# Performance work log

Hardware: AMD Instinct MI355X
Metric: run time of the kernel (lower is better)

Reference implementation:

```python
import jax, jax.numpy as jnp
import numpy as np

ALPHA = 0.5
SMOOTH = 1e-05
ITERS = 10


def _max_pool3x3(x):
    # 3x3 max pool, stride 1, SAME padding on NCHW tensor
    return jax.lax.reduce_window(
        x, -jnp.inf, jax.lax.max,
        window_dimensions=(1, 1, 3, 3),
        window_strides=(1, 1, 1, 1),
        padding='SAME')


def _soft_erode(x):
    return -_max_pool3x3(-x)


def _soft_dilate(x):
    return _max_pool3x3(x)


def _soft_skeletonize(img, iterations=ITERS):
    def body(skel, _):
        eroded = _soft_erode(skel)
        temp = _soft_dilate(eroded)
        skel = skel - (skel - eroded) * temp
        skel = jnp.clip(skel, 0.0, 1.0)
        return skel, None
    skel, _ = jax.lax.scan(body, img, None, length=iterations)
    return skel


def _dice_score(pred, target, smooth=SMOOTH):
    inter = jnp.sum(pred * target, axis=(2, 3))
    union = jnp.sum(pred, axis=(2, 3)) + jnp.sum(target, axis=(2, 3))
    dice = (2.0 * inter + smooth) / (union + smooth)
    return jnp.mean(dice)


def setup_inputs() -> dict:
    key = jax.random.key(0)
    k1, k2 = jax.random.split(key)
    B, C, H, W = 32, 1, 512, 512
    pred_logits = jax.random.normal(k1, (B, C, H, W), dtype=jnp.float32)
    target = jax.random.uniform(k2, (B, C, H, W), dtype=jnp.float32)
    return {"pred_logits": pred_logits, "target": target}


def reference(pred_logits, target):
    pred = jax.nn.sigmoid(pred_logits)
    dice = _dice_score(pred, target)
    pred_skel = _soft_skeletonize(pred)
    target_skel = _soft_skeletonize(target)
    skel_dice = _dice_score(pred_skel, target_skel)
    loss = (1.0 - ALPHA) * (1.0 - dice) + ALPHA * (1.0 - skel_dice)
    return (loss, dice, skel_dice)
```

## Files before the change

kernel.cpp:

```cpp
#include <hip/hip_runtime.h>
#include <hip/hip_fp16.h>
#include <math.h>


#define H 512
#define W 512
#define IMG (H * W)
#define NIMG 64
#define NPRED 32

#define APITCH 80
#define AROWS 74
#define BP2 38
#define BROWS 68

typedef _Float16 f16;
typedef __fp16 fp16v2 __attribute__((ext_vector_type(2)));

__device__ __forceinline__ float2 unpack2(uint u) {
    fp16v2 h = __builtin_bit_cast(fp16v2, u);
    return make_float2((float)h.x, (float)h.y);
}
__device__ __forceinline__ uint pack2(float a, float b) {
    fp16v2 h = __builtin_amdgcn_cvt_pkrtz(a, b);
    return __builtin_bit_cast(uint, h);
}

__device__ __forceinline__ float wsum64(float v) {
#pragma unroll
    for (int o = 32; o > 0; o >>= 1) v += __shfl_down(v, o);
    return v;
}

__device__ __forceinline__ void hmin3(const float* __restrict__ row, float h[6],
                                      float4& q1out) {
    float4 q0 = *(const float4*)(row);
    float4 q1 = *(const float4*)(row + 4);
    float4 q2 = *(const float4*)(row + 8);
    q1out = q1;
    h[0] = fminf(q0.z, fminf(q0.w, q1.x));
    h[1] = fminf(q0.w, fminf(q1.x, q1.y));
    h[2] = fminf(q1.x, fminf(q1.y, q1.z));
    h[3] = fminf(q1.y, fminf(q1.z, q1.w));
    h[4] = fminf(q1.z, fminf(q1.w, q2.x));
    h[5] = fminf(q1.w, fminf(q2.x, q2.y));
}

__device__ __forceinline__ void hmin3h(const uint* __restrict__ row, float h[6],
                                       float4& q1out) {
    uint2 a = *(const uint2*)(row);
    uint2 b = *(const uint2*)(row + 2);
    uint2 d = *(const uint2*)(row + 4);
    float2 p1 = unpack2(a.y);
    float2 p2 = unpack2(b.x);
    float2 p3 = unpack2(b.y);
    float2 p4 = unpack2(d.x);
    q1out = make_float4(p2.x, p2.y, p3.x, p3.y);
    h[0] = fminf(p1.x, fminf(p1.y, p2.x));
    h[1] = fminf(p1.y, fminf(p2.x, p2.y));
    h[2] = fminf(p2.x, fminf(p2.y, p3.x));
    h[3] = fminf(p2.y, fminf(p3.x, p3.y));
    h[4] = fminf(p3.x, fminf(p3.y, p4.x));
    h[5] = fminf(p3.y, fminf(p4.x, p4.y));
}

__device__ __forceinline__ void erode1(const float a[6], const float b[6], const float c[6],
                                       bool rowok, const bool cm[6], float e[6]) {
#pragma unroll
    for (int j = 0; j < 6; j++) {
        float v = fminf(a[j], fminf(b[j], c[j]));
        e[j] = (rowok && cm[j]) ? v : -INFINITY;
    }
}

__device__ __forceinline__ void erode2(const float a[6], const float b[6], const float c[6],
                                       int gy, bool lo, bool ro, float e[6]) {
    bool oob = (gy < 0) || (gy >= H);
#pragma unroll
    for (int j = 0; j < 6; j++) {
        float v = fminf(a[j], fminf(b[j], c[j]));
        e[j] = oob ? -INFINITY : v;
    }
    if (lo) e[0] = -INFINITY;
    if (ro) e[5] = -INFINITY;
}

__device__ __forceinline__ void hmax1(const float e[6], float hx[4], float ec[4]) {
    hx[0] = fmaxf(e[0], fmaxf(e[1], e[2]));
    hx[1] = fmaxf(e[1], fmaxf(e[2], e[3]));
    hx[2] = fmaxf(e[2], fmaxf(e[3], e[4]));
    hx[3] = fmaxf(e[3], fmaxf(e[4], e[5]));
    ec[0] = e[1]; ec[1] = e[2]; ec[2] = e[3]; ec[3] = e[4];
}

template<int SIG>
__device__ void fillA_f32(float* __restrict__ A, const float* __restrict__ src,
                          int tileX, int tileY, int tid) {
    const float PINF = INFINITY;
    for (int it = tid; it < AROWS * 20; it += 256) {
        int r = it / 20;
        int c = it - r * 20;
        int gy = tileY + r - 4;
        int gx = tileX + 4 * c - 8;
        float4 v = make_float4(PINF, PINF, PINF, PINF);
        if ((unsigned)(c - 1) < 18u && (unsigned)gy < (unsigned)H &&
            (unsigned)gx < (unsigned)W) {
            v = *(const float4*)(src + (size_t)gy * W + gx);
            if (SIG) {
                v.x = 1.0f / (1.0f + __expf(-v.x));
                v.y = 1.0f / (1.0f + __expf(-v.y));
                v.z = 1.0f / (1.0f + __expf(-v.z));
                v.w = 1.0f / (1.0f + __expf(-v.w));
            }
        }
        *(float4*)(A + r * APITCH + 4 * c) = v;
    }
}

__device__ void fillA_f16(float* __restrict__ A, const f16* __restrict__ src,
                          int tileX, int tileY, int tid) {
    const float PINF = INFINITY;
    for (int it = tid; it < AROWS * 20; it += 256) {
        int r = it / 20;
        int c = it - r * 20;
        int gy = tileY + r - 4;
        int gx = tileX + 4 * c - 8;
        float4 v = make_float4(PINF, PINF, PINF, PINF);
        if ((unsigned)(c - 1) < 18u && (unsigned)gy < (unsigned)H &&
            (unsigned)gx < (unsigned)W) {
            uint2 g = *(const uint2*)(src + (size_t)gy * W + gx);
            float2 lo = unpack2(g.x), hi = unpack2(g.y);
            v = make_float4(lo.x, lo.y, hi.x, hi.y);
        }
        *(float4*)(A + r * APITCH + 4 * c) = v;
    }
}

__device__ void stage1(const float* __restrict__ A, uint* __restrict__ Bu,
                       int tileX, int tileY, int tid) {
    for (int item = tid; item < 252; item += 256) {
        const int s = item / 18;
        const int q = item - s * 18;
        const int gcb = tileX - 4 + 4 * q;
        const int ys = tileY - 2 + 5 * s;
        bool cm[6], sm[4];
#pragma unroll
        for (int j = 0; j < 6; j++) cm[j] = ((unsigned)(gcb - 1 + j) < (unsigned)W);
#pragma unroll
        for (int j = 0; j < 4; j++) sm[j] = ((unsigned)(gcb + j) < (unsigned)W);
        const int lr = 5 * s + 2;
        const float* Ab = A + 4 * q;
        float hm[3][6], hx[3][4], e[6], ec_cur[4], ec_nxt[4];
        float4 scq[3], qd;
        hmin3(Ab + (lr - 2) * APITCH, hm[0], qd);
        hmin3(Ab + (lr - 1) * APITCH, hm[1], qd);
        hmin3(Ab + (lr + 0) * APITCH, hm[2], scq[0]);
        erode1(hm[0], hm[1], hm[2], (unsigned)(ys - 1) < (unsigned)H, cm, e);
        hmax1(e, hx[0], ec_nxt);
        hmin3(Ab + (lr + 1) * APITCH, hm[0], scq[1]);
        erode1(hm[1], hm[2], hm[0], (unsigned)ys < (unsigned)H, cm, e);
        hmax1(e, hx[1], ec_cur);
#pragma unroll
        for (int k = 0; k < 5; k++) {
            hmin3(Ab + (lr + 2 + k) * APITCH, hm[(k + 1) % 3], scq[(2 + k) % 3]);
            erode1(hm[(k + 2) % 3], hm[k % 3], hm[(k + 1) % 3],
                   (unsigned)(ys + k + 1) < (unsigned)H, cm, e);
            hmax1(e, hx[(k + 2) % 3], ec_nxt);
            float t0 = fmaxf(hx[k % 3][0], fmaxf(hx[(k + 1) % 3][0], hx[(k + 2) % 3][0]));
            float t1 = fmaxf(hx[k % 3][1], fmaxf(hx[(k + 1) % 3][1], hx[(k + 2) % 3][1]));
            float t2 = fmaxf(hx[k % 3][2], fmaxf(hx[(k + 1) % 3][2], hx[(k + 2) % 3][2]));
            float t3 = fmaxf(hx[k % 3][3], fmaxf(hx[(k + 1) % 3][3], hx[(k + 2) % 3][3]));
            float4 sc = scq[k % 3];
            float o0 = fminf(fmaxf(sc.x - (sc.x - ec_cur[0]) * t0, 0.0f), 1.0f);
            float o1 = fminf(fmaxf(sc.y - (sc.y - ec_cur[1]) * t1, 0.0f), 1.0f);
            float o2 = fminf(fmaxf(sc.z - (sc.z - ec_cur[2]) * t2, 0.0f), 1.0f);
            float o3 = fminf(fmaxf(sc.w - (sc.w - ec_cur[3]) * t3, 0.0f), 1.0f);
            int br = 5 * s + k;
            if (br < BROWS) {
                bool rin = ((unsigned)(ys + k) < (unsigned)H);
                float v0 = (rin && sm[0]) ? o0 : INFINITY;
                float v1 = (rin && sm[1]) ? o1 : INFINITY;
                float v2 = (rin && sm[2]) ? o2 : INFINITY;
                float v3 = (rin && sm[3]) ? o3 : INFINITY;
                uint2 wv;
                wv.x = pack2(v0, v1);
                wv.y = pack2(v2, v3);
                *(uint2*)(Bu + br * BP2 + 2 * q) = wv;
            }
            ec_cur[0] = ec_nxt[0]; ec_cur[1] = ec_nxt[1];
            ec_cur[2] = ec_nxt[2]; ec_cur[3] = ec_nxt[3];
        }
    }
}

template<bool TOREG>
__device__ void stage2(const uint* __restrict__ Bu, int tileX, int tileY,
                       int tx, int ty, f16* __restrict__ gdst, float (*oreg)[4]) {
    const int X = tileX + 4 * tx;
    const int gy0 = tileY + 4 * ty;
    const int rb = 4 * ty + 2;
    const bool lo = (X == 0);
    const bool ro = (X + 4 >= W);
    const uint* Bb = Bu + 2 * tx;
    float hm[3][6], hx[3][4], e[6], ec_cur[4], ec_nxt[4];
    float4 scq[3], qd;
    hmin3h(Bb + (rb - 2) * BP2, hm[0], qd);
    hmin3h(Bb + (rb - 1) * BP2, hm[1], qd);
    hmin3h(Bb + (rb + 0) * BP2, hm[2], scq[0]);
    erode2(hm[0], hm[1], hm[2], gy0 - 1, lo, ro, e);
    hmax1(e, hx[0], ec_nxt);
    hmin3h(Bb + (rb + 1) * BP2, hm[0], scq[1]);
    erode2(hm[1], hm[2], hm[0], gy0, lo, ro, e);
    hmax1(e, hx[1], ec_cur);
#pragma unroll
    for (int k = 0; k < 4; k++) {
        hmin3h(Bb + (rb + 2 + k) * BP2, hm[(k + 1) % 3], scq[(2 + k) % 3]);
        erode2(hm[(k + 2) % 3], hm[k % 3], hm[(k + 1) % 3], gy0 + k + 1, lo, ro, e);
        hmax1(e, hx[(k + 2) % 3], ec_nxt);
        float t0 = fmaxf(hx[k % 3][0], fmaxf(hx[(k + 1) % 3][0], hx[(k + 2) % 3][0]));
        float t1 = fmaxf(hx[k % 3][1], fmaxf(hx[(k + 1) % 3][1], hx[(k + 2) % 3][1]));
        float t2 = fmaxf(hx[k % 3][2], fmaxf(hx[(k + 1) % 3][2], hx[(k + 2) % 3][2]));
        float t3 = fmaxf(hx[k % 3][3], fmaxf(hx[(k + 1) % 3][3], hx[(k + 2) % 3][3]));
        float4 sc = scq[k % 3];
        float4 o;
        o.x = fminf(fmaxf(sc.x - (sc.x - ec_cur[0]) * t0, 0.0f), 1.0f);
        o.y = fminf(fmaxf(sc.y - (sc.y - ec_cur[1]) * t1, 0.0f), 1.0f);
        o.z = fminf(fmaxf(sc.z - (sc.z - ec_cur[2]) * t2, 0.0f), 1.0f);
        o.w = fminf(fmaxf(sc.w - (sc.w - ec_cur[3]) * t3, 0.0f), 1.0f);
        if (TOREG) {
            oreg[k][0] = o.x; oreg[k][1] = o.y; oreg[k][2] = o.z; oreg[k][3] = o.w;
        } else {
            uint2 w;
            w.x = pack2(o.x, o.y);
            w.y = pack2(o.z, o.w);
            *(uint2*)(gdst + (size_t)(gy0 + k) * W + X) = w;
        }
        ec_cur[0] = ec_nxt[0]; ec_cur[1] = ec_nxt[1];
        ec_cur[2] = ec_nxt[2]; ec_cur[3] = ec_nxt[3];
    }
}

__global__ __launch_bounds__(256, 4) void k_first(
    const float* __restrict__ logits, const float* __restrict__ target,
    f16* __restrict__ outb, float* __restrict__ parts0, float* __restrict__ parts1) {
    __shared__ float A[AROWS * APITCH];
    __shared__ uint Bu[BROWS * BP2];
    __shared__ float red[8];
    const int img = blockIdx.z;
    const int tileX = blockIdx.x * 64, tileY = blockIdx.y * 64;
    const int tid = threadIdx.y * 16 + threadIdx.x;
    const bool pred = (img < NPRED);
    if (pred) fillA_f32<1>(A, logits + (size_t)img * IMG, tileX, tileY, tid);
    else      fillA_f32<0>(A, target + (size_t)(img - NPRED) * IMG, tileX, tileY, tid);
    __syncthreads();
    float a = 0.0f, b = 0.0f;
    if (pred) {
        const float* tgt = target + (size_t)img * IMG;
        for (int i = tid; i < 1024; i += 256) {
            int r = i >> 4, c4 = (i & 15) * 4;
            float4 p = *(const float4*)(A + (r + 4) * APITCH + c4 + 8);
            float4 t = *(const float4*)(tgt + (size_t)(tileY + r) * W + tileX + c4);
            a += p.x * t.x + p.y * t.y + p.z * t.z + p.w * t.w;
            b += p.x + p.y + p.z + p.w;
        }
    } else {
        for (int i = tid; i < 1024; i += 256) {
            int r = i >> 4, c4 = (i & 15) * 4;
            float4 t = *(const float4*)(A + (r + 4) * APITCH + c4 + 8);
            a += t.x + t.y + t.z + t.w;
        }
    }
    a = wsum64(a); b = wsum64(b);
    if ((tid & 63) == 0) { red[tid >> 6] = a; red[4 + (tid >> 6)] = b; }
    stage1(A, Bu, tileX, tileY, tid);
    __syncthreads();
    if (tid == 0) {
        int bi = blockIdx.z * 64 + blockIdx.y * 8 + blockIdx.x;
        parts0[bi] = red[0] + red[1] + red[2] + red[3];
        parts1[bi] = red[4] + red[5] + red[6] + red[7];
    }
    stage2<false>(Bu, tileX, tileY, threadIdx.x, threadIdx.y,
                  outb + (size_t)img * IMG, nullptr);
}

__global__ __launch_bounds__(256, 4) void k_mid(
    const f16* __restrict__ in, f16* __restrict__ outb) {
    __shared__ float A[AROWS * APITCH];
    __shared__ uint Bu[BROWS * BP2];
    const int img = blockIdx.z;
    const int tileX = blockIdx.x * 64, tileY = blockIdx.y * 64;
    const int tid = threadIdx.y * 16 + threadIdx.x;
    fillA_f16(A, in + (size_t)img * IMG, tileX, tileY, tid);
    __syncthreads();
    stage1(A, Bu, tileX, tileY, tid);
    __syncthreads();
    stage2<false>(Bu, tileX, tileY, threadIdx.x, threadIdx.y,
                  outb + (size_t)img * IMG, nullptr);
}

__global__ __launch_bounds__(256, 4) void k_last(
    const f16* __restrict__ in, float* __restrict__ pA,
    float* __restrict__ pB, float* __restrict__ pC) {
    __shared__ float A[AROWS * APITCH];
    __shared__ uint Bu[BROWS * BP2];
    __shared__ float red[12];
    const int img = blockIdx.z;
    const int tileX = blockIdx.x * 64, tileY = blockIdx.y * 64;
    const int tid = threadIdx.y * 16 + threadIdx.x;
    float op[4][4], ot[4][4];
    fillA_f16(A, in + (size_t)img * IMG, tileX, tileY, tid);
    __syncthreads();
    stage1(A, Bu, tileX, tileY, tid);
    __syncthreads();
    stage2<true>(Bu, tileX, tileY, threadIdx.x, threadIdx.y, nullptr, op);
    fillA_f16(A, in + (size_t)(img + NPRED) * IMG, tileX, tileY, tid);
    __syncthreads();
    stage1(A, Bu, tileX, tileY, tid);
    __syncthreads();
    stage2<true>(Bu, tileX, tileY, threadIdx.x, threadIdx.y, nullptr, ot);
    float a = 0.0f, b = 0.0f, c = 0.0f;
#pragma unroll
    for (int k = 0; k < 4; k++)
#pragma unroll
        for (int j = 0; j < 4; j++) {
            a += op[k][j] * ot[k][j];
            b += op[k][j];
            c += ot[k][j];
        }
    a = wsum64(a); b = wsum64(b); c = wsum64(c);
    if ((tid & 63) == 0) {
        red[tid >> 6] = a; red[4 + (tid >> 6)] = b; red[8 + (tid >> 6)] = c;
    }
    __syncthreads();
    if (tid == 0) {
        int bi = img * 64 + blockIdx.y * 8 + blockIdx.x;
        pA[bi] = red[0] + red[1] + red[2] + red[3];
        pB[bi] = red[4] + red[5] + red[6] + red[7];
        pC[bi] = red[8] + red[9] + red[10] + red[11];
    }
}

__global__ __launch_bounds__(64) void finalize_img(
    const float* __restrict__ parts0, const float* __restrict__ parts1,
    const float* __restrict__ pA, const float* __restrict__ pB,
    const float* __restrict__ pC, float* __restrict__ dices) {
    const int i = blockIdx.x, t = threadIdx.x;
    float inter = wsum64(parts0[i * 64 + t]);
    float sp = wsum64(parts1[i * 64 + t]);
    float st = wsum64(parts0[(NPRED + i) * 64 + t]);
    float i2 = wsum64(pA[i * 64 + t]);
    float sp2 = wsum64(pB[i * 64 + t]);
    float st2 = wsum64(pC[i * 64 + t]);
    if (t == 0) {
        dices[i] = (float)((2.0 * (double)inter + 1e-5) / ((double)sp + (double)st + 1e-5));
        dices[32 + i] = (float)((2.0 * (double)i2 + 1e-5) / ((double)sp2 + (double)st2 + 1e-5));
    }
}

__global__ void finalize_out(const float* __restrict__ dices, float* __restrict__ out) {
    const int t = threadIdx.x;
    double d = 0.0, sd = 0.0;
    if (t < 32) { d = dices[t]; sd = dices[32 + t]; }
#pragma unroll
    for (int o = 32; o > 0; o >>= 1) { d += __shfl_down(d, o); sd += __shfl_down(sd, o); }
    if (t == 0) {
        d *= (1.0 / 32.0); sd *= (1.0 / 32.0);
        out[0] = (float)(0.5 * (1.0 - d) + 0.5 * (1.0 - sd));
        out[1] = (float)d;
        out[2] = (float)sd;
    }
}

extern "C" void kernel_launch(void* const* d_in, const int* in_sizes, int n_in,
                              void* d_out, int out_size, void* d_ws, size_t ws_size,
                              hipStream_t stream) {
    (void)in_sizes; (void)n_in; (void)out_size; (void)ws_size;
    const float* logits = (const float*)d_in[0];
    const float* target = (const float*)d_in[1];
    float* out = (float*)d_out;
    f16* buf0 = (f16*)d_ws;
    f16* buf1 = buf0 + (size_t)NIMG * IMG;
    float* parts0 = (float*)(buf1 + (size_t)NIMG * IMG);
    float* parts1 = parts0 + 4096;
    float* pA = parts1 + 4096;
    float* pB = pA + 2048;
    float* pC = pB + 2048;
    float* dices = pC + 2048;

    dim3 blk(16, 16, 1);
    k_first<<<dim3(8, 8, NIMG), blk, 0, stream>>>(logits, target, buf0, parts0, parts1);
    k_mid<<<dim3(8, 8, NIMG), blk, 0, stream>>>(buf0, buf1);
    k_mid<<<dim3(8, 8, NIMG), blk, 0, stream>>>(buf1, buf0);
    k_mid<<<dim3(8, 8, NIMG), blk, 0, stream>>>(buf0, buf1);
    k_last<<<dim3(8, 8, NPRED), blk, 0, stream>>>(buf1, pA, pB, pC);
    finalize_img<<<32, 64, 0, stream>>>(parts0, parts1, pA, pB, pC, dices);
    finalize_out<<<1, 64, 0, stream>>>(dices, out);
}
```

Baseline: 261.7 us.

## Switch morphology stencil to packed fp16 math with half-size shared tiles

The erode/dilate/update stencil now runs on packed fp16 pairs using v_pk_min/max_f16 and alignbit shifts instead of unpacking to fp32. The shared A tile is stored as fp16 (halving LDS footprint), which lets launch bounds rise from 4 to 6 blocks per SM. The dice partial sums are folded into the first fill loop rather than a separate pass. This cuts ALU and LDS traffic per pixel, but the update arithmetic is now done in fp16, which may change rounding relative to the fp32 path.

Result: no change. 265.6 us (+1.5%).

```diff
diff --git a/kernel.cpp b/kernel.cpp
--- a/kernel.cpp
+++ b/kernel.cpp
@@ -9,186 +9,177 @@
 #define NIMG 64
 #define NPRED 32
 
-#define APITCH 80
+#define APU 40
 #define AROWS 74
 #define BP2 38
 #define BROWS 68
 
+#define PINF2 0x7C007C00u
+#define NINF2 0xFC00FC00u
+#define ONE2  0x3C003C00u
+
 typedef _Float16 f16;
+typedef _Float16 h2 __attribute__((ext_vector_type(2)));
 typedef __fp16 fp16v2 __attribute__((ext_vector_type(2)));
 
-__device__ __forceinline__ float2 unpack2(uint u) {
-    fp16v2 h = __builtin_bit_cast(fp16v2, u);
-    return make_float2((float)h.x, (float)h.y);
-}
 __device__ __forceinline__ uint pack2(float a, float b) {
     fp16v2 h = __builtin_amdgcn_cvt_pkrtz(a, b);
     return __builtin_bit_cast(uint, h);
 }
 
+__device__ __forceinline__ uint pmin(uint a, uint b) {
+    uint d; asm("v_pk_min_f16 %0, %1, %2" : "=v"(d) : "v"(a), "v"(b)); return d;
+}
+__device__ __forceinline__ uint pmax(uint a, uint b) {
+    uint d; asm("v_pk_max_f16 %0, %1, %2" : "=v"(d) : "v"(a), "v"(b)); return d;
+}
+__device__ __forceinline__ uint abit(uint hi, uint lo) {
+    return __builtin_amdgcn_alignbit(hi, lo, 16);
+}
+
 __device__ __forceinline__ float wsum64(float v) {
 #pragma unroll
     for (int o = 32; o > 0; o >>= 1) v += __shfl_down(v, o);
     return v;
 }
 
-__device__ __forceinline__ void hmin3(const float* __restrict__ row, float h[6],
-                                      float4& q1out) {
-    float4 q0 = *(const float4*)(row);
-    float4 q1 = *(const float4*)(row + 4);
-    float4 q2 = *(const float4*)(row + 8);
-    q1out = q1;
-    h[0] = fminf(q0.z, fminf(q0.w, q1.x));
-    h[1] = fminf(q0.w, fminf(q1.x, q1.y));
-    h[2] = fminf(q1.x, fminf(q1.y, q1.z));
-    h[3] = fminf(q1.y, fminf(q1.z, q1.w));
-    h[4] = fminf(q1.z, fminf(q1.w, q2.x));
-    h[5] = fminf(q1.w, fminf(q2.x, q2.y));
-}
-
-__device__ __forceinline__ void hmin3h(const uint* __restrict__ row, float h[6],
-                                       float4& q1out) {
-    uint2 a = *(const uint2*)(row);
-    uint2 b = *(const uint2*)(row + 2);
-    uint2 d = *(const uint2*)(row + 4);
-    float2 p1 = unpack2(a.y);
-    float2 p2 = unpack2(b.x);
-    float2 p3 = unpack2(b.y);
-    float2 p4 = unpack2(d.x);
-    q1out = make_float4(p2.x, p2.y, p3.x, p3.y);
-    h[0] = fminf(p1.x, fminf(p1.y, p2.x));
-    h[1] = fminf(p1.y, fminf(p2.x, p2.y));
-    h[2] = fminf(p2.x, fminf(p2.y, p3.x));
-    h[3] = fminf(p2.y, fminf(p3.x, p3.y));
-    h[4] = fminf(p3.x, fminf(p3.y, p4.x));
-    h[5] = fminf(p3.y, fminf(p4.x, p4.y));
-}
-
-__device__ __forceinline__ void erode1(const float a[6], const float b[6], const float c[6],
-                                       bool rowok, const bool cm[6], float e[6]) {
-#pragma unroll
-    for (int j = 0; j < 6; j++) {
-        float v = fminf(a[j], fminf(b[j], c[j]));
-        e[j] = (rowok && cm[j]) ? v : -INFINITY;
-    }
-}
-
-__device__ __forceinline__ void erode2(const float a[6], const float b[6], const float c[6],
-                                       int gy, bool lo, bool ro, float e[6]) {
-    bool oob = (gy < 0) || (gy >= H);
-#pragma unroll
-    for (int j = 0; j < 6; j++) {
-        float v = fminf(a[j], fminf(b[j], c[j]));
-        e[j] = oob ? -INFINITY : v;
-    }
-    if (lo) e[0] = -INFINITY;
-    if (ro) e[5] = -INFINITY;
-}
-
-__device__ __forceinline__ void hmax1(const float e[6], float hx[4], float ec[4]) {
-    hx[0] = fmaxf(e[0], fmaxf(e[1], e[2]));
-    hx[1] = fmaxf(e[1], fmaxf(e[2], e[3]));
-    hx[2] = fmaxf(e[2], fmaxf(e[3], e[4]));
-    hx[3] = fmaxf(e[3], fmaxf(e[4], e[5]));
-    ec[0] = e[1]; ec[1] = e[2]; ec[2] = e[3]; ec[3] = e[4];
+__device__ __forceinline__ void hmin4p(const uint* __restrict__ p, uint m[4], uint sc[2]) {
+    uint2 w0 = *(const uint2*)(p);
+    uint2 w1 = *(const uint2*)(p + 2);
+    uint2 w2 = *(const uint2*)(p + 4);
+    sc[0] = w1.x; sc[1] = w1.y;
+    uint s01 = abit(w0.y, w0.x);
+    uint s12 = abit(w1.x, w0.y);
+    uint s23 = abit(w1.y, w1.x);
+    uint s34 = abit(w2.x, w1.y);
+    uint s45 = abit(w2.y, w2.x);
+    m[0] = pmin(s01, pmin(w0.y, s12));
+    m[1] = pmin(s12, pmin(w1.x, s23));
+    m[2] = pmin(s23, pmin(w1.y, s34));
+    m[3] = pmin(s34, pmin(w2.x, s45));
+}
+
+__device__ __forceinline__ void erodep(const uint a[4], const uint b[4], const uint c[4],
+                                       bool rowok, const bool eok[4], uint e[4]) {
+#pragma unroll
+    for (int i = 0; i < 4; i++) {
+        uint v = pmin(a[i], pmin(b[i], c[i]));
+        e[i] = (rowok && eok[i]) ? v : NINF2;
+    }
+}
+
+__device__ __forceinline__ void hmaxp(const uint e[4], uint hx[2], uint ec[2]) {
+    uint a12 = abit(e[1], e[0]);
+    uint a23 = abit(e[2], e[1]);
+    uint a34 = abit(e[3], e[2]);
+    hx[0] = pmax(a12, pmax(e[1], a23));
+    hx[1] = pmax(a23, pmax(e[2], a34));
+    ec[0] = e[1]; ec[1] = e[2];
+}
+
+__device__ __forceinline__ uint upd_pair(uint s, uint ec, uint t) {
+    h2 sh = __builtin_bit_cast(h2, s);
+    h2 eh = __builtin_bit_cast(h2, ec);
+    h2 th = __builtin_bit_cast(h2, t);
+    h2 o = sh - (sh - eh) * th;
+    return pmin(pmax(__builtin_bit_cast(uint, o), 0u), ONE2);
 }
 
 template<int SIG>
-__device__ void fillA_f32(float* __restrict__ A, const float* __restrict__ src,
-                          int tileX, int tileY, int tid) {
-    const float PINF = INFINITY;
+__device__ float2 fillA_f32p(uint* __restrict__ A, const float* __restrict__ src,
+                             const float* __restrict__ tgt,
+                             int tileX, int tileY, int tid) {
+    float a = 0.0f, b = 0.0f;
     for (int it = tid; it < AROWS * 20; it += 256) {
         int r = it / 20;
-        int c = it - r * 20;
+        int u2 = it - r * 20;
         int gy = tileY + r - 4;
-        int gx = tileX + 4 * c - 8;
-        float4 v = make_float4(PINF, PINF, PINF, PINF);
-        if ((unsigned)(c - 1) < 18u && (unsigned)gy < (unsigned)H &&
+        int gx = tileX - 8 + 4 * u2;
+        uint2 v = make_uint2(PINF2, PINF2);
+        if (r < 72 && (unsigned)(u2 - 1) < 18u && (unsigned)gy < (unsigned)H &&
             (unsigned)gx < (unsigned)W) {
-            v = *(const float4*)(src + (size_t)gy * W + gx);
+            float4 f = *(const float4*)(src + (size_t)gy * W + gx);
             if (SIG) {
-                v.x = 1.0f / (1.0f + __expf(-v.x));
-                v.y = 1.0f / (1.0f + __expf(-v.y));
-                v.z = 1.0f / (1.0f + __expf(-v.z));
-                v.w = 1.0f / (1.0f + __expf(-v.w));
+                f.x = 1.0f / (1.0f + __expf(-f.x));
+                f.y = 1.0f / (1.0f + __expf(-f.y));
+                f.z = 1.0f / (1.0f + __expf(-f.z));
+                f.w = 1.0f / (1.0f + __expf(-f.w));
             }
-        }
-        *(float4*)(A + r * APITCH + 4 * c) = v;
-    }
-}
-
-__device__ void fillA_f16(float* __restrict__ A, const f16* __restrict__ src,
-                          int tileX, int tileY, int tid) {
-    const float PINF = INFINITY;
+            if (((unsigned)(gx - tileX) < 64u) && ((unsigned)(gy - tileY) < 64u)) {
+                if (SIG) {
+                    float4 t = *(const float4*)(tgt + (size_t)gy * W + gx);
+                    a += f.x * t.x + f.y * t.y + f.z * t.z + f.w * t.w;
+                    b += f.x + f.y + f.z + f.w;
+                } else {
+                    a += f.x + f.y + f.z + f.w;
+                }
+            }
+            v.x = pack2(f.x, f.y);
+            v.y = pack2(f.z, f.w);
+        }
+        *(uint2*)(A + r * APU + 2 * u2) = v;
+    }
+    return make_float2(a, b);
+}
+
+__device__ void fillA_f16p(uint* __restrict__ A, const f16* __restrict__ src,
+                           int tileX, int tileY, int tid) {
     for (int it = tid; it < AROWS * 20; it += 256) {
         int r = it / 20;
-        int c = it - r * 20;
+        int u2 = it - r * 20;
         int gy = tileY + r - 4;
-        int gx = tileX + 4 * c - 8;
-        float4 v = make_float4(PINF, PINF, PINF, PINF);
-        if ((unsigned)(c - 1) < 18u && (unsigned)gy < (unsigned)H &&
+        int gx = tileX - 8 + 4 * u2;
+        uint2 v = make_uint2(PINF2, PINF2);
+        if (r < 72 && (unsigned)(u2 - 1) < 18u && (unsigned)gy < (unsigned)H &&
             (unsigned)gx < (unsigned)W) {
-            uint2 g = *(const uint2*)(src + (size_t)gy * W + gx);
-            float2 lo = unpack2(g.x), hi = unpack2(g.y);
-            v = make_float4(lo.x, lo.y, hi.x, hi.y);
-        }
-        *(float4*)(A + r * APITCH + 4 * c) = v;
-    }
-}
-
-__device__ void stage1(const float* __restrict__ A, uint* __restrict__ Bu,
+            v = *(const uint2*)(src + (size_t)gy * W + gx);
+        }
+        *(uint2*)(A + r * APU + 2 * u2) = v;
+    }
+}
+
+__device__ void stage1(const uint* __restrict__ Au, uint* __restrict__ Bu,
                        int tileX, int tileY, int tid) {
     for (int item = tid; item < 252; item += 256) {
         const int s = item / 18;
         const int q = item - s * 18;
         const int gcb = tileX - 4 + 4 * q;
         const int ys = tileY - 2 + 5 * s;
-        bool cm[6], sm[4];
-#pragma unroll
-        for (int j = 0; j < 6; j++) cm[j] = ((unsigned)(gcb - 1 + j) < (unsigned)W);
-#pragma unroll
-        for (int j = 0; j < 4; j++) sm[j] = ((unsigned)(gcb + j) < (unsigned)W);
+        bool eok[4], wok[2];
+#pragma unroll
+        for (int i = 0; i < 4; i++) eok[i] = ((unsigned)(gcb - 2 + 2 * i) < 511u);
+        wok[0] = ((unsigned)gcb < 511u);
+        wok[1] = ((unsigned)(gcb + 2) < 511u);
         const int lr = 5 * s + 2;
-        const float* Ab = A + 4 * q;
-        float hm[3][6], hx[3][4], e[6], ec_cur[4], ec_nxt[4];
-        float4 scq[3], qd;
-        hmin3(Ab + (lr - 2) * APITCH, hm[0], qd);
-        hmin3(Ab + (lr - 1) * APITCH, hm[1], qd);
-        hmin3(Ab + (lr + 0) * APITCH, hm[2], scq[0]);
-        erode1(hm[0], hm[1], hm[2], (unsigned)(ys - 1) < (unsigned)H, cm, e);
-        hmax1(e, hx[0], ec_nxt);
-        hmin3(Ab + (lr + 1) * APITCH, hm[0], scq[1]);
-        erode1(hm[1], hm[2], hm[0], (unsigned)ys < (unsigned)H, cm, e);
-        hmax1(e, hx[1], ec_cur);
+        const uint* Ab = Au + 2 * q;
+        uint m[3][4], sc[3][2], hx[3][2], e[4], ec_cur[2], ec_nxt[2], tsc[2];
+        hmin4p(Ab + (lr - 2) * APU, m[0], tsc);
+        hmin4p(Ab + (lr - 1) * APU, m[1], tsc);
+        hmin4p(Ab + (lr + 0) * APU, m[2], sc[0]);
+        erodep(m[0], m[1], m[2], (unsigned)(ys - 1) < (unsigned)H, eok, e);
+        hmaxp(e, hx[0], ec_nxt);
+        hmin4p(Ab + (lr + 1) * APU, m[0], sc[1]);
+        erodep(m[1], m[2], m[0], (unsigned)ys < (unsigned)H, eok, e);
+        hmaxp(e, hx[1], ec_cur);
 #pragma unroll
         for (int k = 0; k < 5; k++) {
-            hmin3(Ab + (lr + 2 + k) * APITCH, hm[(k + 1) % 3], scq[(2 + k) % 3]);
-            erode1(hm[(k + 2) % 3], hm[k % 3], hm[(k + 1) % 3],
-                   (unsigned)(ys + k + 1) < (unsigned)H, cm, e);
-            hmax1(e, hx[(k + 2) % 3], ec_nxt);
-            float t0 = fmaxf(hx[k % 3][0], fmaxf(hx[(k + 1) % 3][0], hx[(k + 2) % 3][0]));
-            float t1 = fmaxf(hx[k % 3][1], fmaxf(hx[(k + 1) % 3][1], hx[(k + 2) % 3][1]));
-            float t2 = fmaxf(hx[k % 3][2], fmaxf(hx[(k + 1) % 3][2], hx[(k + 2) % 3][2]));
-            float t3 = fmaxf(hx[k % 3][3], fmaxf(hx[(k + 1) % 3][3], hx[(k + 2) % 3][3]));
-            float4 sc = scq[k % 3];
-            float o0 = fminf(fmaxf(sc.x - (sc.x - ec_cur[0]) * t0, 0.0f), 1.0f);
-            float o1 = fminf(fmaxf(sc.y - (sc.y - ec_cur[1]) * t1, 0.0f), 1.0f);
-            float o2 = fminf(fmaxf(sc.z - (sc.z - ec_cur[2]) * t2, 0.0f), 1.0f);
-            float o3 = fminf(fmaxf(sc.w - (sc.w - ec_cur[3]) * t3, 0.0f), 1.0f);
+            hmin4p(Ab + (lr + 2 + k) * APU, m[(k + 1) % 3], sc[(2 + k) % 3]);
+            erodep(m[(k + 2) % 3], m[k % 3], m[(k + 1) % 3],
+                   (unsigned)(ys + k + 1) < (unsigned)H, eok, e);
+            hmaxp(e, hx[(k + 2) % 3], ec_nxt);
             int br = 5 * s + k;
             if (br < BROWS) {
+                uint t0 = pmax(hx[k % 3][0], pmax(hx[(k + 1) % 3][0], hx[(k + 2) % 3][0]));
+                uint t1 = pmax(hx[k % 3][1], pmax(hx[(k + 1) % 3][1], hx[(k + 2) % 3][1]));
+                uint o0 = upd_pair(sc[k % 3][0], ec_cur[0], t0);
+                uint o1 = upd_pair(sc[k % 3][1], ec_cur[1], t1);
                 bool rin = ((unsigned)(ys + k) < (unsigned)H);
-                float v0 = (rin && sm[0]) ? o0 : INFINITY;
-                float v1 = (rin && sm[1]) ? o1 : INFINITY;
-                float v2 = (rin && sm[2]) ? o2 : INFINITY;
-                float v3 = (rin && sm[3]) ? o3 : INFINITY;
                 uint2 wv;
-                wv.x = pack2(v0, v1);
-                wv.y = pack2(v2, v3);
+                wv.x = (rin && wok[0]) ? o0 : PINF2;
+                wv.y = (rin && wok[1]) ? o1 : PINF2;
                 *(uint2*)(Bu + br * BP2 + 2 * q) = wv;
             }
             ec_cur[0] = ec_nxt[0]; ec_cur[1] = ec_nxt[1];
-            ec_cur[2] = ec_nxt[2]; ec_cur[3] = ec_nxt[3];
         }
     }
 }
@@ -199,78 +190,60 @@
     const int X = tileX + 4 * tx;
     const int gy0 = tileY + 4 * ty;
     const int rb = 4 * ty + 2;
-    const bool lo = (X == 0);
-    const bool ro = (X + 4 >= W);
+    bool eok[4];
+    eok[0] = (X != 0);
+    eok[1] = true;
+    eok[2] = true;
+    eok[3] = (X + 4 < W);
     const uint* Bb = Bu + 2 * tx;
-    float hm[3][6], hx[3][4], e[6], ec_cur[4], ec_nxt[4];
-    float4 scq[3], qd;
-    hmin3h(Bb + (rb - 2) * BP2, hm[0], qd);
-    hmin3h(Bb + (rb - 1) * BP2, hm[1], qd);
-    hmin3h(Bb + (rb + 0) * BP2, hm[2], scq[0]);
-    erode2(hm[0], hm[1], hm[2], gy0 - 1, lo, ro, e);
-    hmax1(e, hx[0], ec_nxt);
-    hmin3h(Bb + (rb + 1) * BP2, hm[0], scq[1]);
-    erode2(hm[1], hm[2], hm[0], gy0, lo, ro, e);
-    hmax1(e, hx[1], ec_cur);
+    uint m[3][4], sc[3][2], hx[3][2], e[4], ec_cur[2], ec_nxt[2], tsc[2];
+    hmin4p(Bb + (rb - 2) * BP2, m[0], tsc);
+    hmin4p(Bb + (rb - 1) * BP2, m[1], tsc);
+    hmin4p(Bb + (rb + 0) * BP2, m[2], sc[0]);
+    erodep(m[0], m[1], m[2], (unsigned)(gy0 - 1) < (unsigned)H, eok, e);
+    hmaxp(e, hx[0], ec_nxt);
+    hmin4p(Bb + (rb + 1) * BP2, m[0], sc[1]);
+    erodep(m[1], m[2], m[0], true, eok, e);
+    hmaxp(e, hx[1], ec_cur);
 #pragma unroll
     for (int k = 0; k < 4; k++) {
-        hmin3h(Bb + (rb + 2 + k) * BP2, hm[(k + 1) % 3], scq[(2 + k) % 3]);
-        erode2(hm[(k + 2) % 3], hm[k % 3], hm[(k + 1) % 3], gy0 + k + 1, lo, ro, e);
-        hmax1(e, hx[(k + 2) % 3], ec_nxt);
-        float t0 = fmaxf(hx[k % 3][0], fmaxf(hx[(k + 1) % 3][0], hx[(k + 2) % 3][0]));
-        float t1 = fmaxf(hx[k % 3][1], fmaxf(hx[(k + 1) % 3][1], hx[(k + 2) % 3][1]));
-        float t2 = fmaxf(hx[k % 3][2], fmaxf(hx[(k + 1) % 3][2], hx[(k + 2) % 3][2]));
-        float t3 = fmaxf(hx[k % 3][3], fmaxf(hx[(k + 1) % 3][3], hx[(k + 2) % 3][3]));
-        float4 sc = scq[k % 3];
-        float4 o;
-        o.x = fminf(fmaxf(sc.x - (sc.x - ec_cur[0]) * t0, 0.0f), 1.0f);
-        o.y = fminf(fmaxf(sc.y - (sc.y - ec_cur[1]) * t1, 0.0f), 1.0f);
-        o.z = fminf(fmaxf(sc.z - (sc.z - ec_cur[2]) * t2, 0.0f), 1.0f);
-        o.w = fminf(fmaxf(sc.w - (sc.w - ec_cur[3]) * t3, 0.0f), 1.0f);
+        hmin4p(Bb + (rb + 2 + k) * BP2, m[(k + 1) % 3], sc[(2 + k) % 3]);
+        erodep(m[(k + 2) % 3], m[k % 3], m[(k + 1) % 3],
+               (unsigned)(gy0 + k + 1) < (unsigned)H, eok, e);
+        hmaxp(e, hx[(k + 2) % 3], ec_nxt);
+        uint t0 = pmax(hx[k % 3][0], pmax(hx[(k + 1) % 3][0], hx[(k + 2) % 3][0]));
+        uint t1 = pmax(hx[k % 3][1], pmax(hx[(k + 1) % 3][1], hx[(k + 2) % 3][1]));
+        uint o0 = upd_pair(sc[k % 3][0], ec_cur[0], t0);
+        uint o1 = upd_pair(sc[k % 3][1], ec_cur[1], t1);
         if (TOREG) {
-            oreg[k][0] = o.x; oreg[k][1] = o.y; oreg[k][2] = o.z; oreg[k][3] = o.w;
+            h2 a = __builtin_bit_cast(h2, o0);
+            h2 b = __builtin_bit_cast(h2, o1);
+            oreg[k][0] = (float)a.x; oreg[k][1] = (float)a.y;
+            oreg[k][2] = (float)b.x; oreg[k][3] = (float)b.y;
         } else {
-            uint2 w;
-            w.x = pack2(o.x, o.y);
-            w.y = pack2(o.z, o.w);
-            *(uint2*)(gdst + (size_t)(gy0 + k) * W + X) = w;
+            *(uint2*)(gdst + (size_t)(gy0 + k) * W + X) = make_uint2(o0, o1);
         }
         ec_cur[0] = ec_nxt[0]; ec_cur[1] = ec_nxt[1];
-        ec_cur[2] = ec_nxt[2]; ec_cur[3] = ec_nxt[3];
-    }
-}
-
-__global__ __launch_bounds__(256, 4) void k_first(
+    }
+}
+
+__global__ __launch_bounds__(256, 6) void k_first(
     const float* __restrict__ logits, const float* __restrict__ target,
     f16* __restrict__ outb, float* __restrict__ parts0, float* __restrict__ parts1) {
-    __shared__ float A[AROWS * APITCH];
-    __shared__ uint Bu[BROWS * BP2];
+    __shared__ __align__(16) uint A[AROWS * APU];
+    __shared__ __align__(16) uint Bu[BROWS * BP2];
     __shared__ float red[8];
     const int img = blockIdx.z;
     const int tileX = blockIdx.x * 64, tileY = blockIdx.y * 64;
     const int tid = threadIdx.y * 16 + threadIdx.x;
     const bool pred = (img < NPRED);
-    if (pred) fillA_f32<1>(A, logits + (size_t)img * IMG, tileX, tileY, tid);
-    else      fillA_f32<0>(A, target + (size_t)(img - NPRED) * IMG, tileX, tileY, tid);
-    __syncthreads();
-    float a = 0.0f, b = 0.0f;
-    if (pred) {
-        const float* tgt = target + (size_t)img * IMG;
-        for (int i = tid; i < 1024; i += 256) {
-            int r = i >> 4, c4 = (i & 15) * 4;
-            float4 p = *(const float4*)(A + (r + 4) * APITCH + c4 + 8);
-            float4 t = *(const float4*)(tgt + (size_t)(tileY + r) * W + tileX + c4);
-            a += p.x * t.x + p.y * t.y + p.z * t.z + p.w * t.w;
-            b += p.x + p.y + p.z + p.w;
-        }
-    } else {
-        for (int i = tid; i < 1024; i += 256) {
-            int r = i >> 4, c4 = (i & 15) * 4;
-            float4 t = *(const float4*)(A + (r + 4) * APITCH + c4 + 8);
-            a += t.x + t.y + t.z + t.w;
-        }
-    }
-    a = wsum64(a); b = wsum64(b);
+    float2 ab;
+    if (pred) ab = fillA_f32p<1>(A, logits + (size_t)img * IMG,
+                                 target + (size_t)img * IMG, tileX, tileY, tid);
+    else      ab = fillA_f32p<0>(A, target + (size_t)(img - NPRED) * IMG,
+                                 nullptr, tileX, tileY, tid);
+    __syncthreads();
+    float a = wsum64(ab.x), b = wsum64(ab.y);
     if ((tid & 63) == 0) { red[tid >> 6] = a; red[4 + (tid >> 6)] = b; }
     stage1(A, Bu, tileX, tileY, tid);
     __syncthreads();
@@ -283,14 +256,14 @@
                   outb + (size_t)img * IMG, nullptr);
 }
 
-__global__ __launch_bounds__(256, 4) void k_mid(
+__global__ __launch_bounds__(256, 6) void k_mid(
     const f16* __restrict__ in, f16* __restrict__ outb) {
-    __shared__ float A[AROWS * APITCH];
-    __shared__ uint Bu[BROWS * BP2];
+    __shared__ __align__(16) uint A[AROWS * APU];
+    __shared__ __align__(16) uint Bu[BROWS * BP2];
     const int img = blockIdx.z;
     const int tileX = blockIdx.x * 64, tileY = blockIdx.y * 64;
     const int tid = threadIdx.y * 16 + threadIdx.x;
-    fillA_f16(A, in + (size_t)img * IMG, tileX, tileY, tid);
+    fillA_f16p(A, in + (size_t)img * IMG, tileX, tileY, tid);
     __syncthreads();
     stage1(A, Bu, tileX, tileY, tid);
     __syncthreads();
@@ -298,22 +271,22 @@
                   outb + (size_t)img * IMG, nullptr);
 }
 
-__global__ __launch_bounds__(256, 4) void k_last(
+__global__ __launch_bounds__(256, 6) void k_last(
     const f16* __restrict__ in, float* __restrict__ pA,
     float* __restrict__ pB, float* __restrict__ pC) {
-    __shared__ float A[AROWS * APITCH];
-    __shared__ uint Bu[BROWS * BP2];
+    __shared__ __align__(16) uint A[AROWS * APU];
+    __shared__ __align__(16) uint Bu[BROWS * BP2];
     __shared__ float red[12];
     const int img = blockIdx.z;
     const int tileX = blockIdx.x * 64, tileY = blockIdx.y * 64;
     const int tid = threadIdx.y * 16 + threadIdx.x;
     float op[4][4], ot[4][4];
-    fillA_f16(A, in + (size_t)img * IMG, tileX, tileY, tid);
+    fillA_f16p(A, in + (size_t)img * IMG, tileX, tileY, tid);
     __syncthreads();
     stage1(A, Bu, tileX, tileY, tid);
     __syncthreads();
     stage2<true>(Bu, tileX, tileY, threadIdx.x, threadIdx.y, nullptr, op);
-    fillA_f16(A, in + (size_t)(img + NPRED) * IMG, tileX, tileY, tid);
+    fillA_f16p(A, in + (size_t)(img + NPRED) * IMG, tileX, tileY, tid);
     __syncthreads();
     stage1(A, Bu, tileX, tileY, tid);
     __syncthreads();
```
